# Optimization experiments

Hardware: AMD Instinct MI355X
Metric: run time of the kernel (lower is better)

Reference implementation:

```python
import jax, jax.numpy as jnp
import numpy as np

D_MODEL = 1024
NUM_HEADS = 16
D_K = D_MODEL // NUM_HEADS


def setup_inputs() -> dict:
    key = jax.random.key(0)
    ks = jax.random.split(key, 11)
    B, S = 2, 2048
    scale = 1.0 / np.sqrt(D_MODEL)
    inp = {
        'q': jax.random.normal(ks[0], (B, S, D_MODEL), jnp.float32),
        'k': jax.random.normal(ks[1], (B, S, D_MODEL), jnp.float32),
        'v': jax.random.normal(ks[2], (B, S, D_MODEL), jnp.float32),
        'Wq': jax.random.normal(ks[3], (D_MODEL, D_MODEL), jnp.float32) * scale,
        'bq': jnp.zeros((D_MODEL,), jnp.float32),
        'Wk': jax.random.normal(ks[4], (D_MODEL, D_MODEL), jnp.float32) * scale,
        'bk': jnp.zeros((D_MODEL,), jnp.float32),
        'Wv': jax.random.normal(ks[5], (D_MODEL, D_MODEL), jnp.float32) * scale,
        'bv': jnp.zeros((D_MODEL,), jnp.float32),
        'Wo': jax.random.normal(ks[6], (D_MODEL, D_MODEL), jnp.float32) * scale,
        'bo': jnp.zeros((D_MODEL,), jnp.float32),
    }
    return inp


def _split_heads(x):
    # [B, S, d_model] -> [B, H, S, d_k]
    B, S, _ = x.shape
    return x.reshape(B, S, NUM_HEADS, D_K).transpose(0, 2, 1, 3)


def reference(q, k, v, Wq, bq, Wk, bk, Wv, bv, Wo, bo):
    B, S, _ = q.shape
    qh = _split_heads(q @ Wq + bq)
    kh = _split_heads(k @ Wk + bk)
    vh = _split_heads(v @ Wv + bv)
    scores = jnp.einsum('bhsd,bhtd->bhst', qh, kh) / np.sqrt(D_K)
    attn = jax.nn.softmax(scores, axis=-1)  # dropout is identity in eval
    out = jnp.einsum('bhst,bhtd->bhsd', attn, vh)
    out = out.transpose(0, 2, 1, 3).reshape(B, S, D_MODEL)
    return out @ Wo + bo
```

## Files before the change

kernel.cpp:

```cpp
#include <hip/hip_runtime.h>

typedef unsigned short u16;
typedef unsigned int u32;
typedef __attribute__((ext_vector_type(4))) float f32x4;
typedef __attribute__((ext_vector_type(16))) float f32x16;
typedef __attribute__((ext_vector_type(8))) short bf16x8;
typedef __attribute__((ext_vector_type(4))) unsigned short u16x4;
typedef __attribute__((ext_vector_type(8))) unsigned short u16x8;
typedef __attribute__((ext_vector_type(4))) unsigned int u32x4;

#define S_LEN 2048
#define DMODEL 1024

__device__ __forceinline__ u16 f2bf(float f) {
  union { float f; unsigned int i; } c; c.f = f;
  unsigned int v = c.i + 0x7FFFu + ((c.i >> 16) & 1u);
  return (u16)(v >> 16);
}
__device__ __forceinline__ u32 cvtpk(float lo, float hi) {
  u32 r;
  asm("v_cvt_pk_bf16_f32 %0, %1, %2" : "=v"(r) : "v"(lo), "v"(hi));
  return r;
}
__device__ __forceinline__ float exp2v(float x) {
  float r;
  asm("v_exp_f32 %0, %1" : "=v"(r) : "v"(x));
  return r;
}

typedef const __attribute__((address_space(1))) void gv_t;
typedef __attribute__((address_space(3))) void lv_t;
__device__ __forceinline__ void gload_lds16(const void* g, void* l) {
  __builtin_amdgcn_global_load_lds((gv_t*)g, (lv_t*)l, 16, 0, 0);
}

#define LGKM0 do { asm volatile("s_waitcnt lgkmcnt(0)" ::: "memory"); __builtin_amdgcn_sched_barrier(0); } while (0)
#define VMC4  do { asm volatile("s_waitcnt vmcnt(4)" ::: "memory"); __builtin_amdgcn_sched_barrier(0); } while (0)
#define BAR   __builtin_amdgcn_s_barrier()

__global__ __launch_bounds__(256) void k_cvt3(const float* __restrict__ s0,
                                              const float* __restrict__ s1,
                                              const float* __restrict__ s2,
                                              u16* __restrict__ d0,
                                              u16* __restrict__ d1,
                                              u16* __restrict__ d2) {
  int i = blockIdx.x * 256 + threadIdx.x;
  int seg = i >> 19, idx = i & 524287;
  const float* s = seg == 0 ? s0 : (seg == 1 ? s1 : s2);
  u16* d = seg == 0 ? d0 : (seg == 1 ? d1 : d2);
  f32x4 a = ((const f32x4*)s)[idx * 2];
  f32x4 b = ((const f32x4*)s)[idx * 2 + 1];
  u16x8 o;
#pragma unroll
  for (int j = 0; j < 4; ++j) { o[j] = f2bf(a[j]); o[j + 4] = f2bf(b[j]); }
  ((u16x8*)d)[idx] = o;
}

struct TwArgs { const float* src[4]; u16* dst[4]; };
__global__ __launch_bounds__(256) void k_twcvt4(TwArgs ta) {
  __shared__ u16 tile[64][68];
  int wsel = blockIdx.x >> 8;
  int bx = blockIdx.x & 255;
  const float* src = ta.src[wsel];
  u16* dst = ta.dst[wsel];
  const int R = 1024, C = 1024;
  int tr = bx >> 4, tc = bx & 15;
  int r0 = tr << 6, c0 = tc << 6;
  int t = threadIdx.x;
#pragma unroll
  for (int i = 0; i < 4; ++i) {
    int e = (t + i * 256) << 2;
    int rr = e >> 6, cc = e & 63;
    f32x4 v = *(const f32x4*)&src[(size_t)(r0 + rr) * C + (c0 + cc)];
#pragma unroll
    for (int j = 0; j < 4; ++j) tile[rr][cc + j] = f2bf(v[j]);
  }
  __syncthreads();
#pragma unroll
  for (int i = 0; i < 4; ++i) {
    int e = (t + i * 256) << 2;
    int rr = e >> 6, cc = e & 63;
    u16x4 v;
#pragma unroll
    for (int j = 0; j < 4; ++j) v[j] = tile[cc + j][rr];
    *(u16x4*)&dst[(size_t)(c0 + rr) * R + (r0 + cc)] = v;
  }
}

__global__ __launch_bounds__(256) void k_pack(const u16* __restrict__ Ck,
                                              const u16* __restrict__ Cv,
                                              u16* __restrict__ Kp,
                                              u16* __restrict__ Vp) {
  int bx = blockIdx.x;
  if (bx < 2048) {
    int flat = bx * 256 + threadIdx.x;
    int lane = flat & 63, kd = (flat >> 6) & 3, kt = (flat >> 8) & 63;
    int h = (flat >> 14) & 15, b = flat >> 18;
    int l31 = lane & 31, hi = lane >> 5;
    const u16* src = &Ck[(size_t)(b * 2048 + kt * 32 + l31) * 1024 + h * 64 + kd * 16 + hi * 8];
    ((u16x8*)Kp)[flat] = *(const u16x8*)src;
  } else {
    int flat = (bx - 2048) * 256 + threadIdx.x;
    int lane = flat & 63, ks = (flat >> 6) & 3, dvh = (flat >> 8) & 1;
    int kt = (flat >> 9) & 31, h = (flat >> 14) & 15, b = flat >> 18;
    int l31 = lane & 31, hi = lane >> 5;
    const u16* src = &Cv[(size_t)(b * 2048 + kt * 64 + ks * 16 + hi * 8) * 1024 + h * 64 + dvh * 32 + l31];
    u16x8 o;
#pragma unroll
    for (int j = 0; j < 8; ++j) o[j] = src[(size_t)j * 1024];
    ((u16x8*)Vp)[flat] = o;
  }
}

struct GemmSet { const u16* A; const u16* Bt; const float* bias; void* C; };
struct GemmArgs { GemmSet s[3]; };

template <int MB>
__device__ __forceinline__ void quad16(f32x4 (&acc)[8][4], const bf16x8 (&Af)[4],
                                       const bf16x8 (&Bf)[4]) {
#pragma unroll
  for (int mi = 0; mi < 4; ++mi)
#pragma unroll
    for (int nf = 0; nf < 4; ++nf)
      acc[MB + mi][nf] = __builtin_amdgcn_mfma_f32_16x16x32_bf16(Af[mi], Bf[nf],
                                                                 acc[MB + mi][nf], 0, 0, 0);
}
template <int MB>
__device__ __forceinline__ void rda4(bf16x8 (&Af)[4], const char* base, const int (&aoff)[8]) {
#pragma unroll
  for (int mi = 0; mi < 4; ++mi) Af[mi] = *(const bf16x8*)(base + aoff[MB + mi]);
}
__device__ __forceinline__ void rdb4(bf16x8 (&Bf)[4], const char* base, const int (&boff)[4]) {
#pragma unroll
  for (int nf = 0; nf < 4; ++nf) Bf[nf] = *(const bf16x8*)(base + boff[nf]);
}

__global__ __launch_bounds__(512, 2) void k_gemm8(GemmArgs ga) {
  __shared__ __align__(16) u16 lds[2][2][2][256 * 32];
  int tid = threadIdx.x;
  int lane = tid & 63, w = tid >> 6;
  int cl = lane & 15, g = lane >> 4;
  int wr = w >> 2, wc = w & 3;
  int wgs = ((blockIdx.x & 7) * 24) + (blockIdx.x >> 3);
  int mat = wgs >> 6;
  int rr = wgs & 63;
  int m0 = (rr >> 2) << 8, n0 = (rr & 3) << 8;
  const u16* A = ga.s[mat].A;
  const u16* Bt = ga.s[mat].Bt;

  int srow[2], scol[2];
#pragma unroll
  for (int i = 0; i < 2; ++i) {
    int c = tid + i * 512;
    int cp = c ^ (((c >> 5) & 3) << 1);
    srow[i] = cp >> 2;
    scol[i] = (cp & 3) * 8;
  }
  int aoff[8], boff[4];
#pragma unroll
  for (int mf = 0; mf < 8; ++mf) {
    int x = (wr * 128 + mf * 16 + cl) * 64 + g * 16;
    aoff[mf] = x ^ (((x >> 9) & 3) << 5);
  }
#pragma unroll
  for (int nf = 0; nf < 4; ++nf) {
    int x = (wc * 64 + nf * 16 + cl) * 64 + g * 16;
    boff[nf] = x ^ (((x >> 9) & 3) << 5);
  }

  f32x4 acc[8][4];
  f32x4 z4 = {0.f, 0.f, 0.f, 0.f};
#pragma unroll
  for (int i = 0; i < 8; ++i)
#pragma unroll
    for (int j = 0; j < 4; ++j) acc[i][j] = z4;

  auto STAGE = [&](int u, int ab, int hk) {
    int k0 = (u << 6) + (hk << 5);
    const u16* src = ab ? Bt : A;
    int rb = ab ? n0 : m0;
    u16* dst = &lds[u & 1][ab][hk][0];
#pragma unroll
    for (int i = 0; i < 2; ++i)
      gload_lds16(&src[(size_t)(rb + srow[i]) * 1024 + k0 + scol[i]],
                  &dst[(w * 64 + i * 512) * 8]);
  };

  STAGE(0, 0, 0); STAGE(0, 1, 0); STAGE(0, 0, 1); STAGE(0, 1, 1);
  VMC4;
  BAR;

  bf16x8 Af[4], Bf[4];
#pragma unroll 2
  for (int t = 0; t < 16; ++t) {
    int d = t & 1;
    int u = t + 1;
    bool st = u < 16;
    const char* Ah0 = (const char*)&lds[d][0][0][0];
    const char* Bh0 = (const char*)&lds[d][1][0][0];
    const char* Ah1 = (const char*)&lds[d][0][1][0];
    const char* Bh1 = (const char*)&lds[d][1][1][0];
    rda4<0>(Af, Ah0, aoff); rdb4(Bf, Bh0, boff);
    if (st) STAGE(u, 0, 0);
    BAR; LGKM0;
    __builtin_amdgcn_s_setprio(1); quad16<0>(acc, Af, Bf); __builtin_amdgcn_s_setprio(0);
    BAR;
    rda4<4>(Af, Ah0, aoff);
    if (st) STAGE(u, 1, 0);
    BAR; LGKM0;
    __builtin_amdgcn_s_setprio(1); quad16<4>(acc, Af, Bf); __builtin_amdgcn_s_setprio(0);
    VMC4;
    BAR;
    rda4<0>(Af, Ah1, aoff); rdb4(Bf, Bh1, boff);
    if (st) STAGE(u, 0, 1);
    BAR; LGKM0;
    __builtin_amdgcn_s_setprio(1); quad16<0>(acc, Af, Bf); __builtin_amdgcn_s_setprio(0);
    BAR;
    rda4<4>(Af, Ah1, aoff);
    if (st) STAGE(u, 1, 1);
    BAR; LGKM0;
    __builtin_amdgcn_s_setprio(1); quad16<4>(acc, Af, Bf); __builtin_amdgcn_s_setprio(0);
    VMC4;
    BAR;
  }

  const float* bias = ga.s[mat].bias;
  u16* C = (u16*)ga.s[mat].C;
#pragma unroll
  for (int nf = 0; nf < 4; ++nf) {
    int n = n0 + wc * 64 + nf * 16 + cl;
    float bv = bias[n];
#pragma unroll
    for (int mf = 0; mf < 8; ++mf) {
      int row0 = m0 + wr * 128 + mf * 16 + g * 4;
#pragma unroll
      for (int j = 0; j < 4; ++j)
        C[(size_t)(row0 + j) * 1024 + n] = f2bf(acc[mf][nf][j] + bv);
    }
  }
}

__global__ __launch_bounds__(256) void k_gemm_out(const u16* __restrict__ A,
                                                  const u16* __restrict__ Bt,
                                                  const float* __restrict__ bias,
                                                  float* __restrict__ C) {
  constexpr int K = 1024, N = 1024;
  __shared__ __align__(16) u16 Al[128 * 32];
  __shared__ __align__(16) u16 Bl[128 * 32];
  int t = blockIdx.x;
  int m0 = (t & 31) << 7;
  int n0 = (t >> 5) << 7;
  int lane = threadIdx.x & 63, w = threadIdx.x >> 6;
  int g = lane >> 4, cl = lane & 15;
  int wr = w >> 1, wc = w & 1;
  f32x4 zero4 = {0.f, 0.f, 0.f, 0.f};
  f32x4 acc[4][4];
#pragma unroll
  for (int i = 0; i < 4; ++i)
#pragma unroll
    for (int j = 0; j < 4; ++j) acc[i][j] = zero4;

  int srow0 = w * 32 + (lane >> 2);
  int scol = (lane & 3) << 3;
  for (int kt = 0; kt < K / 32; ++kt) {
    int k0 = kt << 5;
#pragma unroll
    for (int c = 0; c < 2; ++c) {
      int row = srow0 + c * 16;
      gload_lds16(&A[(size_t)(m0 + row) * K + k0 + scol], &Al[w * 1024 + c * 512]);
      gload_lds16(&Bt[(size_t)(n0 + row) * K + k0 + scol], &Bl[w * 1024 + c * 512]);
    }
    __syncthreads();
    bf16x8 af[4], bfm[4];
#pragma unroll
    for (int i = 0; i < 4; ++i) {
      af[i]  = *(const bf16x8*)&Al[(wr * 64 + i * 16 + cl) * 32 + g * 8];
      bfm[i] = *(const bf16x8*)&Bl[(wc * 64 + i * 16 + cl) * 32 + g * 8];
    }
#pragma unroll
    for (int mi = 0; mi < 4; ++mi)
#pragma unroll
      for (int ni = 0; ni < 4; ++ni)
        acc[mi][ni] = __builtin_amdgcn_mfma_f32_16x16x32_bf16(af[mi], bfm[ni], acc[mi][ni], 0, 0, 0);
    __syncthreads();
  }
#pragma unroll
  for (int ni = 0; ni < 4; ++ni) {
    int n = n0 + wc * 64 + ni * 16 + cl;
    float bv = bias[n];
#pragma unroll
    for (int mi = 0; mi < 4; ++mi) {
      int r0 = m0 + wr * 64 + mi * 16 + g * 4;
#pragma unroll
      for (int r = 0; r < 4; ++r)
        C[(size_t)(r0 + r) * N + n] = acc[mi][ni][r] + bv;
    }
  }
}

__global__ __launch_bounds__(256, 4) void k_attn5(const u16* __restrict__ Q,
                                                  const u16* __restrict__ Kp,
                                                  const u16* __restrict__ Vp,
                                                  u16* __restrict__ O) {
  __shared__ __align__(16) float Ol[2][32][64];
  __shared__ float Ml[2][32];
  int lane = threadIdx.x & 63, w = threadIdx.x >> 6;
  int l31 = lane & 31, hi = lane >> 5;
  int half = w >> 1, sub = w & 1;
  int bx = blockIdx.x;
  int logical = (bx & 7) * 128 + (bx >> 3);
  int bh = logical >> 5, qblk = logical & 31;
  int b = bh >> 4, h = bh & 15;
  const u16* Qb = Q + (size_t)b * S_LEN * DMODEL + h * 64;
  const u16* Kph = Kp + (size_t)(b * 16 + h) * (64 * 4 * 64 * 8);
  const u16* Vph = Vp + (size_t)(b * 16 + h) * (32 * 2 * 4 * 64 * 8);
  u16* Ob = O + (size_t)b * S_LEN * DMODEL + h * 64;
  int qbase = qblk * 64 + sub * 32;

  bf16x8 qf[4];
  const u16* qp = &Qb[(size_t)(qbase + l31) * DMODEL + hi * 8];
#pragma unroll
  for (int kd = 0; kd < 4; ++kd) qf[kd] = *(const bf16x8*)&qp[kd * 16];

  f32x16 zero16 = {0};
  f32x16 oa0 = zero16, oa1 = zero16;
  float lsum = 0.f;
  const float C2 = 0.125f * 1.44269504f;
  const float MC2 = 64.0f * C2;

  int kt0 = half * 16;
  for (int kt = kt0; kt < kt0 + 16; ++kt) {
    const u16* kpt = Kph + (size_t)kt * 4096 + (size_t)lane * 8;
    const u16* vpt = Vph + (size_t)kt * 4096 + (size_t)lane * 8;

    f32x16 s0 = zero16, s1 = zero16;
    __builtin_amdgcn_s_setprio(1);
#pragma unroll
    for (int kd = 0; kd < 4; ++kd) {
      bf16x8 kfa = *(const bf16x8*)&kpt[kd * 512];
      bf16x8 kfb = *(const bf16x8*)&kpt[2048 + kd * 512];
      s0 = __builtin_amdgcn_mfma_f32_32x32x16_bf16(kfa, qf[kd], s0, 0, 0, 0);
      s1 = __builtin_amdgcn_mfma_f32_32x32x16_bf16(kfb, qf[kd], s1, 0, 0, 0);
    }
    __builtin_amdgcn_s_setprio(0);

    bf16x8 vf0[4], vf1[4];
#pragma unroll
    for (int ks = 0; ks < 4; ++ks) {
      vf0[ks] = *(const bf16x8*)&vpt[ks * 512];
      vf1[ks] = *(const bf16x8*)&vpt[2048 + ks * 512];
    }

    float rs = 0.f;
    bf16x8 af[4];
#pragma unroll
    for (int tile = 0; tile < 2; ++tile) {
      const f32x16& sv = tile ? s1 : s0;
#pragma unroll
      for (int hq = 0; hq < 2; ++hq) {
        float p0 = exp2v(__builtin_fmaf(sv[hq * 8 + 0], C2, -MC2));
        float p1 = exp2v(__builtin_fmaf(sv[hq * 8 + 1], C2, -MC2));
        rs += p0 + p1;
        u32 w0 = cvtpk(p0, p1);
        p0 = exp2v(__builtin_fmaf(sv[hq * 8 + 2], C2, -MC2));
        p1 = exp2v(__builtin_fmaf(sv[hq * 8 + 3], C2, -MC2));
        rs += p0 + p1;
        u32 w1 = cvtpk(p0, p1);
        p0 = exp2v(__builtin_fmaf(sv[hq * 8 + 4], C2, -MC2));
        p1 = exp2v(__builtin_fmaf(sv[hq * 8 + 5], C2, -MC2));
        rs += p0 + p1;
        u32 w2 = cvtpk(p0, p1);
        p0 = exp2v(__builtin_fmaf(sv[hq * 8 + 6], C2, -MC2));
        p1 = exp2v(__builtin_fmaf(sv[hq * 8 + 7], C2, -MC2));
        rs += p0 + p1;
        u32 w3 = cvtpk(p0, p1);
        u32 x0 = __shfl_xor(w0, 32, 64), x1 = __shfl_xor(w1, 32, 64);
        u32 x2 = __shfl_xor(w2, 32, 64), x3 = __shfl_xor(w3, 32, 64);
        union { u32x4 u; bf16x8 v; } c;
        c.u = u32x4{hi ? x2 : w0, hi ? x3 : w1, hi ? w2 : x0, hi ? w3 : x1};
        af[tile * 2 + hq] = c.v;
      }
    }
    lsum += rs + __shfl_xor(rs, 32, 64);

    __builtin_amdgcn_s_setprio(1);
#pragma unroll
    for (int ks = 0; ks < 4; ++ks) {
      oa0 = __builtin_amdgcn_mfma_f32_32x32x16_bf16(af[ks], vf0[ks], oa0, 0, 0, 0);
      oa1 = __builtin_amdgcn_mfma_f32_32x32x16_bf16(af[ks], vf1[ks], oa1, 0, 0, 0);
    }
    __builtin_amdgcn_s_setprio(0);
  }

  if (half == 1) {
#pragma unroll
    for (int r = 0; r < 16; ++r) {
      int q = ((r & 3) + 8 * (r >> 2)) + 4 * hi;
      Ol[sub][q][l31] = oa0[r];
      Ol[sub][q][l31 + 32] = oa1[r];
    }
    if (hi == 0) Ml[sub][l31] = lsum;
  }
  __syncthreads();
  if (half == 0) {
    float invl = 1.0f / (lsum + Ml[sub][l31]);
#pragma unroll
    for (int r = 0; r < 16; ++r) {
      int q = ((r & 3) + 8 * (r >> 2)) + 4 * hi;
      float f0 = __shfl(invl, q, 64);
      int row = qbase + q;
      float o0 = (oa0[r] + Ol[sub][q][l31]) * f0;
      float o1 = (oa1[r] + Ol[sub][q][l31 + 32]) * f0;
      Ob[(size_t)row * DMODEL + l31]      = f2bf(o0);
      Ob[(size_t)row * DMODEL + 32 + l31] = f2bf(o1);
    }
  }
}

extern "C" void kernel_launch(void* const* d_in, const int* in_sizes, int n_in,
                              void* d_out, int out_size, void* d_ws, size_t ws_size,
                              hipStream_t stream) {
  const float* q  = (const float*)d_in[0];
  const float* k  = (const float*)d_in[1];
  const float* v  = (const float*)d_in[2];
  const float* Wq = (const float*)d_in[3];
  const float* bq = (const float*)d_in[4];
  const float* Wk = (const float*)d_in[5];
  const float* bk = (const float*)d_in[6];
  const float* Wv = (const float*)d_in[7];
  const float* bv = (const float*)d_in[8];
  const float* Wo = (const float*)d_in[9];
  const float* bo = (const float*)d_in[10];
  float* out = (float*)d_out;
  char* ws = (char*)d_ws;
  const size_t MB = 1024 * 1024;
  u16* wtq = (u16*)(ws + 0 * MB);
  u16* wtk = (u16*)(ws + 2 * MB);
  u16* wtv = (u16*)(ws + 4 * MB);
  u16* wto = (u16*)(ws + 6 * MB);
  u16* qb  = (u16*)(ws + 8 * MB);
  u16* kb  = (u16*)(ws + 16 * MB);
  u16* vb  = (u16*)(ws + 24 * MB);
  u16* Cq  = (u16*)(ws + 32 * MB);
  u16* Ck  = (u16*)(ws + 40 * MB);
  u16* Cv  = (u16*)(ws + 48 * MB);
  u16* Kp  = qb;
  u16* Vp  = vb;
  u16* O   = kb;

  k_cvt3<<<6144, 256, 0, stream>>>(q, k, v, qb, kb, vb);

  TwArgs ta;
  ta.src[0] = Wq; ta.src[1] = Wk; ta.src[2] = Wv; ta.src[3] = Wo;
  ta.dst[0] = wtq; ta.dst[1] = wtk; ta.dst[2] = wtv; ta.dst[3] = wto;
  k_twcvt4<<<1024, 256, 0, stream>>>(ta);

  GemmArgs ga;
  ga.s[0] = {qb, wtq, bq, (void*)Cq};
  ga.s[1] = {kb, wtk, bk, (void*)Ck};
  ga.s[2] = {vb, wtv, bv, (void*)Cv};
  k_gemm8<<<192, 512, 0, stream>>>(ga);

  k_pack<<<4096, 256, 0, stream>>>(Ck, Cv, Kp, Vp);

  k_attn5<<<1024, 256, 0, stream>>>(Cq, Kp, Vp, O);

  k_gemm_out<<<256, 256, 0, stream>>>(O, wto, bo, out);
}
```

Baseline: 246.1 us.

## Remap blocks to XCDs for L2 locality and widen output GEMM to 8 waves

Remaps the block index in the K/V pack kernel and the fused QKV GEMM so blocks that share rows or heads land on the same XCD, aiming for better L2 reuse. The output projection GEMM moves from 4 to 8 waves per block with a 2x4 wave grid, each wave handling 64x32. It also adds an XOR swizzle on the LDS layout to cut bank conflicts and issues one staging load per thread. In exchange, each wave does fewer MFMAs per LDS read, and the new index mappings must still cover every tile exactly once.

After: 245.0 us. No clear change (-0.5%).

```diff
diff --git a/kernel.cpp b/kernel.cpp
--- a/kernel.cpp
+++ b/kernel.cpp
@@ -93,14 +93,23 @@
                                               u16* __restrict__ Vp) {
   int bx = blockIdx.x;
   if (bx < 2048) {
-    int flat = bx * 256 + threadIdx.x;
+    int xcd = bx & 7;
+    int idx = bx >> 3;
+    int bhp = xcd * 4 + (idx >> 6);
+    int within = idx & 63;
+    int flat = (bhp * 64 + within) * 256 + threadIdx.x;
     int lane = flat & 63, kd = (flat >> 6) & 3, kt = (flat >> 8) & 63;
     int h = (flat >> 14) & 15, b = flat >> 18;
     int l31 = lane & 31, hi = lane >> 5;
     const u16* src = &Ck[(size_t)(b * 2048 + kt * 32 + l31) * 1024 + h * 64 + kd * 16 + hi * 8];
     ((u16x8*)Kp)[flat] = *(const u16x8*)src;
   } else {
-    int flat = (bx - 2048) * 256 + threadIdx.x;
+    int bx2 = bx - 2048;
+    int xcd = bx2 & 7;
+    int idx = bx2 >> 3;
+    int bhp = xcd * 4 + (idx >> 6);
+    int within = idx & 63;
+    int flat = (bhp * 64 + within) * 256 + threadIdx.x;
     int lane = flat & 63, ks = (flat >> 6) & 3, dvh = (flat >> 8) & 1;
     int kt = (flat >> 9) & 31, h = (flat >> 14) & 15, b = flat >> 18;
     int l31 = lane & 31, hi = lane >> 5;
@@ -141,10 +150,13 @@
   int lane = tid & 63, w = tid >> 6;
   int cl = lane & 15, g = lane >> 4;
   int wr = w >> 2, wc = w & 3;
-  int wgs = ((blockIdx.x & 7) * 24) + (blockIdx.x >> 3);
-  int mat = wgs >> 6;
-  int rr = wgs & 63;
-  int m0 = (rr >> 2) << 8, n0 = (rr & 3) << 8;
+  int xcd = blockIdx.x & 7;
+  int j6 = blockIdx.x >> 3;
+  int mat = j6 >> 3;
+  int mt = j6 & 7;
+  int bb = xcd >> 2;
+  int ng = xcd & 3;
+  int m0 = (bb * 8 + mt) << 8, n0 = ng << 8;
   const u16* A = ga.s[mat].A;
   const u16* Bt = ga.s[mat].Bt;
 
@@ -240,7 +252,7 @@
   }
 }
 
-__global__ __launch_bounds__(256) void k_gemm_out(const u16* __restrict__ A,
+__global__ __launch_bounds__(512) void k_gemm_out(const u16* __restrict__ A,
                                                   const u16* __restrict__ Bt,
                                                   const float* __restrict__ bias,
                                                   float* __restrict__ C) {
@@ -248,45 +260,55 @@
   __shared__ __align__(16) u16 Al[128 * 32];
   __shared__ __align__(16) u16 Bl[128 * 32];
   int t = blockIdx.x;
-  int m0 = (t & 31) << 7;
-  int n0 = (t >> 5) << 7;
-  int lane = threadIdx.x & 63, w = threadIdx.x >> 6;
+  int m0 = (t >> 3) << 7;
+  int n0 = (t & 7) << 7;
+  int tid = threadIdx.x;
+  int lane = tid & 63, w = tid >> 6;
   int g = lane >> 4, cl = lane & 15;
-  int wr = w >> 1, wc = w & 1;
+  int wr = w >> 2, wc = w & 3;
+
+  int cp = tid ^ ((tid >> 3) & 3);
+  int srow = cp >> 2;
+  int scol = (cp & 3) << 3;
+  int aoff[4], boff[2];
+#pragma unroll
+  for (int mi = 0; mi < 4; ++mi) {
+    int x = (wr * 64 + mi * 16 + cl) * 64 + g * 16;
+    aoff[mi] = x ^ (((x >> 7) & 3) << 4);
+  }
+#pragma unroll
+  for (int ni = 0; ni < 2; ++ni) {
+    int x = (wc * 32 + ni * 16 + cl) * 64 + g * 16;
+    boff[ni] = x ^ (((x >> 7) & 3) << 4);
+  }
+
   f32x4 zero4 = {0.f, 0.f, 0.f, 0.f};
-  f32x4 acc[4][4];
+  f32x4 acc[4][2];
 #pragma unroll
   for (int i = 0; i < 4; ++i)
 #pragma unroll
-    for (int j = 0; j < 4; ++j) acc[i][j] = zero4;
-
-  int srow0 = w * 32 + (lane >> 2);
-  int scol = (lane & 3) << 3;
+    for (int j = 0; j < 2; ++j) acc[i][j] = zero4;
+
   for (int kt = 0; kt < K / 32; ++kt) {
     int k0 = kt << 5;
-#pragma unroll
-    for (int c = 0; c < 2; ++c) {
-      int row = srow0 + c * 16;
-      gload_lds16(&A[(size_t)(m0 + row) * K + k0 + scol], &Al[w * 1024 + c * 512]);
-      gload_lds16(&Bt[(size_t)(n0 + row) * K + k0 + scol], &Bl[w * 1024 + c * 512]);
-    }
+    gload_lds16(&A[(size_t)(m0 + srow) * K + k0 + scol], &Al[(w * 64) * 8]);
+    gload_lds16(&Bt[(size_t)(n0 + srow) * K + k0 + scol], &Bl[(w * 64) * 8]);
     __syncthreads();
-    bf16x8 af[4], bfm[4];
-#pragma unroll
-    for (int i = 0; i < 4; ++i) {
-      af[i]  = *(const bf16x8*)&Al[(wr * 64 + i * 16 + cl) * 32 + g * 8];
-      bfm[i] = *(const bf16x8*)&Bl[(wc * 64 + i * 16 + cl) * 32 + g * 8];
-    }
+    bf16x8 af[4], bfm[2];
+#pragma unroll
+    for (int mi = 0; mi < 4; ++mi) af[mi] = *(const bf16x8*)((const char*)Al + aoff[mi]);
+#pragma unroll
+    for (int ni = 0; ni < 2; ++ni) bfm[ni] = *(const bf16x8*)((const char*)Bl + boff[ni]);
 #pragma unroll
     for (int mi = 0; mi < 4; ++mi)
 #pragma unroll
-      for (int ni = 0; ni < 4; ++ni)
+      for (int ni = 0; ni < 2; ++ni)
         acc[mi][ni] = __builtin_amdgcn_mfma_f32_16x16x32_bf16(af[mi], bfm[ni], acc[mi][ni], 0, 0, 0);
     __syncthreads();
   }
 #pragma unroll
-  for (int ni = 0; ni < 4; ++ni) {
-    int n = n0 + wc * 64 + ni * 16 + cl;
+  for (int ni = 0; ni < 2; ++ni) {
+    int n = n0 + wc * 32 + ni * 16 + cl;
     float bv = bias[n];
 #pragma unroll
     for (int mi = 0; mi < 4; ++mi) {
@@ -465,5 +487,5 @@
 
   k_attn5<<<1024, 256, 0, stream>>>(Cq, Kp, Vp, O);
 
-  k_gemm_out<<<256, 256, 0, stream>>>(O, wto, bo, out);
-}
+  k_gemm_out<<<256, 512, 0, stream>>>(O, wto, bo, out);
+}
```
